# Kernel tuning notes

Measured on AMD Instinct MI355X. Metric: run time of the kernel, lower is better.

## Reference

```python
import jax, jax.numpy as jnp
import numpy as np

B, S, D, H = 4, 2048, 1024, 16
DK = D // H


def setup_inputs() -> dict:
    key = jax.random.key(0)
    ks = jax.random.split(key, 12)
    std = 0.02
    inp = {
        "q": jax.random.normal(ks[0], (B, S, D), jnp.float32),
        "k": jax.random.normal(ks[1], (B, S, D), jnp.float32),
        "v": jax.random.normal(ks[2], (B, S, D), jnp.float32),
        # causal mask: 1 above diagonal (positions to be masked with -inf)
        "mask": jnp.triu(jnp.ones((S, S), jnp.int32), k=1)[None, None, :, :],
        "Wq": jax.random.normal(ks[3], (D, D), jnp.float32) * std,
        "bq": jnp.zeros((D,), jnp.float32),
        "Wk": jax.random.normal(ks[4], (D, D), jnp.float32) * std,
        "bk": jnp.zeros((D,), jnp.float32),
        "Wv": jax.random.normal(ks[5], (D, D), jnp.float32) * std,
        "bv": jnp.zeros((D,), jnp.float32),
        "Wo": jax.random.normal(ks[6], (D, D), jnp.float32) * std,
        "bo": jnp.zeros((D,), jnp.float32),
    }
    return inp


def _split_heads(x):
    b, s, d = x.shape
    return x.reshape(b, s, H, DK).transpose(0, 2, 1, 3)  # [B,H,S,DK]


def reference(q, k, v, mask, Wq, bq, Wk, bk, Wv, bv, Wo, bo):
    # linear projections (torch Linear: x @ W.T + b)
    qh = _split_heads(q @ Wq.T + bq)
    kh = _split_heads(k @ Wk.T + bk)
    vh = _split_heads(v @ Wv.T + bv)
    scale = 1.0 / jnp.sqrt(jnp.asarray(DK, qh.dtype))
    scores = jnp.einsum("bhqd,bhkd->bhqk", qh, kh) * scale
    scores = jnp.where(mask == 1, -jnp.inf, scores)
    attn = jax.nn.softmax(scores, axis=-1)
    # dropout is identity in eval mode (deterministic reference)
    out = jnp.einsum("bhqk,bhkd->bhqd", attn, vh)
    concat = out.transpose(0, 2, 1, 3).reshape(q.shape[0], -1, D)
    return concat @ Wo.T + bo
```

## Files before the change

kernel.cpp:

```cpp
#include <hip/hip_runtime.h>
#include <hip/hip_bf16.h>

#define BB  4
#define SS  2048
#define DD  1024
#define HH  16
#define DKK 64

typedef unsigned short u16;
typedef short v8s __attribute__((ext_vector_type(8)));
typedef short v4s __attribute__((ext_vector_type(4)));
typedef float v4f __attribute__((ext_vector_type(4)));
typedef float v16f __attribute__((ext_vector_type(16)));
typedef unsigned int v4u __attribute__((ext_vector_type(4)));

#define MFMA32(a, b, c) __builtin_amdgcn_mfma_f32_32x32x16_bf16(a, b, c, 0, 0, 0)

__device__ __forceinline__ u16 f2b(float x) {
  unsigned int u = __float_as_uint(x);
  unsigned int r = (u + 0x7fffu + ((u >> 16) & 1u)) >> 16;
  return (u16)r;
}

__device__ __forceinline__ unsigned int pkhalf(float a, float b) {
  return __builtin_amdgcn_perm(__float_as_uint(a), __float_as_uint(b), 0x03020706u);
}

__device__ __forceinline__ void gload16(const u16* g, u16* l) {
  __builtin_amdgcn_global_load_lds(
      (const __attribute__((address_space(1))) void*)g,
      (__attribute__((address_space(3))) void*)l, 16, 0, 0);
}

__device__ __forceinline__ void cvt8(const float* in, u16* out, size_t j) {
  const float4* p = (const float4*)(in + j * 8);
  float4 a = p[0], b = p[1];
  v8s r = {(short)f2b(a.x), (short)f2b(a.y), (short)f2b(a.z), (short)f2b(a.w),
           (short)f2b(b.x), (short)f2b(b.y), (short)f2b(b.z), (short)f2b(b.w)};
  *(v8s*)(out + j * 8) = r;
}

__global__ void cvt3(const float* __restrict__ q, const float* __restrict__ k,
                     const float* __restrict__ v, u16* __restrict__ x0,
                     u16* __restrict__ x1, u16* __restrict__ x2) {
  int i = blockIdx.x * blockDim.x + threadIdx.x;
  int which = i >> 20;
  size_t j = (size_t)(i & 0xFFFFF);
  const float* s = which == 0 ? q : (which == 1 ? k : v);
  u16* d = which == 0 ? x0 : (which == 1 ? x1 : x2);
  cvt8(s, d, j);
}

__global__ void cvtW(const float* __restrict__ a, const float* __restrict__ b,
                     const float* __restrict__ c, const float* __restrict__ d,
                     u16* __restrict__ oa, u16* __restrict__ ob,
                     u16* __restrict__ oc, u16* __restrict__ od) {
  int i = blockIdx.x * blockDim.x + threadIdx.x;
  int which = i >> 17;
  size_t j = (size_t)(i & 0x1FFFF);
  const float* s = which == 0 ? a : (which == 1 ? b : (which == 2 ? c : d));
  u16* o = which == 0 ? oa : (which == 1 ? ob : (which == 2 ? oc : od));
  cvt8(s, o, j);
}

__device__ __forceinline__ void gemm_core32(
    const u16* __restrict__ A, const u16* __restrict__ Bw,
    int row0, int col0, u16* As, u16* Bs, v4f acc[4][4]) {
  const int tid = threadIdx.x;
  const int lane = tid & 63, wid = tid >> 6;
  const int wm = wid >> 1, wn = wid & 1;
  const int lr = lane & 15, lg = lane >> 4;

  v4f zero = {0.f, 0.f, 0.f, 0.f};
#pragma unroll
  for (int m = 0; m < 4; ++m)
#pragma unroll
    for (int n = 0; n < 4; ++n) acc[m][n] = zero;

  const int srow = wid * 16 + (lane >> 2);
  const int scol = ((lane & 3) ^ ((lane >> 3) & 3)) * 8;
  const u16* gA = A + (size_t)(row0 + srow) * DD + scol;
  const u16* gB = Bw + (size_t)(col0 + srow) * DD + scol;
  u16* lA = As + wid * 512;
  u16* lB = Bs + wid * 512;

#pragma unroll
  for (int i2 = 0; i2 < 2; ++i2) {
    gload16(gA + (size_t)(i2 * 64) * DD, lA + i2 * 2048);
    gload16(gB + (size_t)(i2 * 64) * DD, lB + i2 * 2048);
  }
  asm volatile("s_waitcnt vmcnt(0)" ::: "memory");
  __builtin_amdgcn_s_barrier();

  const int aswz = (lg ^ ((lr >> 1) & 3)) * 8;

  for (int t = 0; t < 32; ++t) {
    const int buf = t & 1;
    if (t < 31) {
#pragma unroll
      for (int i2 = 0; i2 < 2; ++i2) {
        gload16(gA + (size_t)(i2 * 64) * DD + (t + 1) * 32,
                lA + (buf ^ 1) * 4096 + i2 * 2048);
        gload16(gB + (size_t)(i2 * 64) * DD + (t + 1) * 32,
                lB + (buf ^ 1) * 4096 + i2 * 2048);
      }
    }
    const u16* Ab = As + buf * 4096;
    const u16* Bb = Bs + buf * 4096;
    v8s af[4], bf[4];
#pragma unroll
    for (int m = 0; m < 4; ++m)
      af[m] = *(const v8s*)(Ab + (wm * 64 + m * 16 + lr) * 32 + aswz);
#pragma unroll
    for (int n = 0; n < 4; ++n)
      bf[n] = *(const v8s*)(Bb + (wn * 64 + n * 16 + lr) * 32 + aswz);
#pragma unroll
    for (int m = 0; m < 4; ++m)
#pragma unroll
      for (int n = 0; n < 4; ++n)
        acc[m][n] = __builtin_amdgcn_mfma_f32_16x16x32_bf16(af[m], bf[n], acc[m][n], 0, 0, 0);

    asm volatile("s_waitcnt vmcnt(0)" ::: "memory");
    __builtin_amdgcn_s_barrier();
  }
}

__global__ __launch_bounds__(256) void gemm_qkv(
    const u16* __restrict__ X0, const u16* __restrict__ X1, const u16* __restrict__ X2,
    const u16* __restrict__ Wqb, const u16* __restrict__ Wkb, const u16* __restrict__ Wvb,
    const float* __restrict__ bq, const float* __restrict__ bk, const float* __restrict__ bv,
    u16* __restrict__ Qp, u16* __restrict__ Kp, u16* __restrict__ VT, float qsc) {
  __shared__ u16 As[2][128][32];
  __shared__ u16 Bs[2][128][32];
  const int z = blockIdx.z;
  const u16* A = z == 0 ? X0 : (z == 1 ? X1 : X2);
  const u16* Bw = z == 0 ? Wqb : (z == 1 ? Wkb : Wvb);
  const float* bias = z == 0 ? bq : (z == 1 ? bk : bv);
  const float oscale = z == 0 ? qsc : 1.0f;
  const int row0 = blockIdx.x * 128, col0 = blockIdx.y * 128;

  v4f acc[4][4];
  gemm_core32(A, Bw, row0, col0, &As[0][0][0], &Bs[0][0][0], acc);

  const int tid = threadIdx.x;
  const int lane = tid & 63, wid = tid >> 6;
  const int wm = wid >> 1, wn = wid & 1;
  const int lr = lane & 15, lg = lane >> 4;

  if (z < 2) {
    u16* C = z == 0 ? Qp : Kp;
#pragma unroll
    for (int n = 0; n < 4; ++n) {
      int gc = col0 + wn * 64 + n * 16 + lr;
      float bv2 = bias[gc];
#pragma unroll
      for (int m = 0; m < 4; ++m) {
        int gr0 = row0 + wm * 64 + m * 16 + lg * 4;
#pragma unroll
        for (int r = 0; r < 4; ++r)
          C[(size_t)(gr0 + r) * DD + gc] = f2b((acc[m][n][r] + bv2) * oscale);
      }
    }
  } else {
#pragma unroll
    for (int n = 0; n < 4; ++n) {
      int gc = col0 + wn * 64 + n * 16 + lr;
      float bv2 = bias[gc];
      int h = gc >> 6, dk = gc & 63;
#pragma unroll
      for (int m = 0; m < 4; ++m) {
        int gr0 = row0 + wm * 64 + m * 16 + lg * 4;
        int b = gr0 >> 11;
        int s = gr0 & 2047;
        u16* vbase = VT + (((size_t)b * HH + h) * DKK + dk) * SS + s;
#pragma unroll
        for (int r = 0; r < 4; ++r) vbase[r] = f2b(acc[m][n][r] + bv2);
      }
    }
  }
}

__global__ __launch_bounds__(256) void gemm_out(
    const u16* __restrict__ A, const u16* __restrict__ Bw,
    const float* __restrict__ bias, float* __restrict__ Cp) {
  __shared__ u16 As[2][128][32];
  __shared__ u16 Bs[2][128][32];
  const int row0 = blockIdx.x * 128, col0 = blockIdx.y * 128;

  v4f acc[4][4];
  gemm_core32(A, Bw, row0, col0, &As[0][0][0], &Bs[0][0][0], acc);

  const int tid = threadIdx.x;
  const int lane = tid & 63, wid = tid >> 6;
  const int wm = wid >> 1, wn = wid & 1;
  const int lr = lane & 15, lg = lane >> 4;

#pragma unroll
  for (int n = 0; n < 4; ++n) {
    int gc = col0 + wn * 64 + n * 16 + lr;
    float bv2 = bias[gc];
#pragma unroll
    for (int m = 0; m < 4; ++m) {
      int gr0 = row0 + wm * 64 + m * 16 + lg * 4;
#pragma unroll
      for (int r = 0; r < 4; ++r)
        Cp[(size_t)(gr0 + r) * DD + gc] = acc[m][n][r] + bv2;
    }
  }
}

__device__ __forceinline__ void build_pa(const v16f& p, int hi, v8s& a0, v8s& a1) {
  unsigned int u0 = pkhalf(p[0], p[1]);
  unsigned int u1 = pkhalf(p[2], p[3]);
  unsigned int u2 = pkhalf(p[4], p[5]);
  unsigned int u3 = pkhalf(p[6], p[7]);
  unsigned int u4 = pkhalf(p[8], p[9]);
  unsigned int u5 = pkhalf(p[10], p[11]);
  unsigned int u6 = pkhalf(p[12], p[13]);
  unsigned int u7 = pkhalf(p[14], p[15]);
  unsigned int s0 = hi ? u0 : u2;
  unsigned int s1 = hi ? u1 : u3;
  unsigned int s2 = hi ? u4 : u6;
  unsigned int s3 = hi ? u5 : u7;
  unsigned int r0 = __shfl_xor(s0, 32);
  unsigned int r1 = __shfl_xor(s1, 32);
  unsigned int r2 = __shfl_xor(s2, 32);
  unsigned int r3 = __shfl_xor(s3, 32);
  v4u f0 = {hi ? r0 : u0, hi ? r1 : u1, hi ? u2 : r0, hi ? u3 : r1};
  v4u f1 = {hi ? r2 : u4, hi ? r3 : u5, hi ? u6 : r2, hi ? u7 : r3};
  a0 = __builtin_bit_cast(v8s, f0);
  a1 = __builtin_bit_cast(v8s, f1);
}

__global__ __launch_bounds__(256) void attn_fwd5(
    const u16* __restrict__ Qp, const u16* __restrict__ Kp,
    const u16* __restrict__ VT, u16* __restrict__ O) {
  __shared__ u16 Ks[128][72];
  __shared__ u16 Vs[64][136];
  const int tid = threadIdx.x;
  const int w = tid >> 6, lane = tid & 63;
  const int ql = lane & 31;
  const int hi = lane >> 5;
  const int i = blockIdx.x;
  const int dw = i >> 8, sl2 = i & 255;
  const int bh = sl2 & 63, g = sl2 >> 6;
  const int qt = (int)((0x3210674598BACDEFull >> (4 * (dw * 4 + g))) & 15);
  const int b = bh >> 4, h = bh & 15;
  const int q0 = qt * 128;
  const int qw0 = q0 + w * 32;
  const int qg = qw0 + ql;

  v8s qf[4];
  const u16* qbase = Qp + (size_t)(b * SS + qg) * DD + h * DKK + hi * 8;
#pragma unroll
  for (int ks = 0; ks < 4; ++ks) qf[ks] = *(const v8s*)(qbase + ks * 16);

  const int krow = tid >> 3, kcol = (tid & 7) * 8;
  const int vrow = tid >> 4, vcol = (tid & 15) * 8;
  const u16* gK = Kp + (size_t)(b * SS + krow) * DD + h * DKK + kcol;
  const u16* gV = VT + ((size_t)bh * DKK + vrow) * SS + vcol;

  const int nt = qt + 1;
  v8s stK[4], stV[4];
#pragma unroll
  for (int j = 0; j < 4; ++j) stK[j] = *(const v8s*)(gK + (size_t)(32 * j) * DD);
#pragma unroll
  for (int j = 0; j < 4; ++j) stV[j] = *(const v8s*)(gV + (size_t)(16 * j) * SS);

  float l = 0.f;
  v16f o0 = {0, 0, 0, 0, 0, 0, 0, 0, 0, 0, 0, 0, 0, 0, 0, 0};
  v16f o1 = o0;

  for (int t = 0; t < nt; ++t) {
    __syncthreads();
#pragma unroll
    for (int j = 0; j < 4; ++j) *(v8s*)&Ks[krow + 32 * j][kcol] = stK[j];
#pragma unroll
    for (int j = 0; j < 4; ++j) *(v8s*)&Vs[vrow + 16 * j][vcol] = stV[j];
    if (t + 1 < nt) {
      const u16* nK = gK + (size_t)(t + 1) * 128 * DD;
      const u16* nV = gV + (t + 1) * 128;
#pragma unroll
      for (int j = 0; j < 4; ++j) stK[j] = *(const v8s*)(nK + (size_t)(32 * j) * DD);
#pragma unroll
      for (int j = 0; j < 4; ++j) stV[j] = *(const v8s*)(nV + (size_t)(16 * j) * SS);
    }
    __syncthreads();
    const int kv0 = t * 128;

#pragma unroll
    for (int sub = 0; sub < 4; ++sub) {
      const int kvs = kv0 + sub * 32;
      if (kvs > qw0 + 31) break;

      v16f p = {0, 0, 0, 0, 0, 0, 0, 0, 0, 0, 0, 0, 0, 0, 0, 0};
#pragma unroll
      for (int ks = 0; ks < 4; ++ks) {
        v8s a = *(const v8s*)&Ks[sub * 32 + ql][ks * 16 + hi * 8];
        p = MFMA32(a, qf[ks], p);
      }

      if (kvs + 31 > qw0) {
#pragma unroll
        for (int r = 0; r < 16; ++r) {
          int row = (r & 3) + 8 * (r >> 2) + 4 * hi;
          if (kvs + row > qg) p[r] = -3.0e38f;
        }
      }

      float rs = 0.f;
#pragma unroll
      for (int r = 0; r < 16; ++r) {
        p[r] = exp2f(p[r]);
        rs += p[r];
      }
      l += rs;

      v8s pa0, pa1;
      build_pa(p, hi, pa0, pa1);

      __builtin_amdgcn_s_setprio(1);
      o0 = MFMA32(pa0, *(const v8s*)&Vs[ql][sub * 32 + hi * 8], o0);
      o0 = MFMA32(pa1, *(const v8s*)&Vs[ql][sub * 32 + 16 + hi * 8], o0);
      o1 = MFMA32(pa0, *(const v8s*)&Vs[32 + ql][sub * 32 + hi * 8], o1);
      o1 = MFMA32(pa1, *(const v8s*)&Vs[32 + ql][sub * 32 + 16 + hi * 8], o1);
      __builtin_amdgcn_s_setprio(0);
    }
  }

  float lt = l + __shfl_xor(l, 32);
  float linv = 1.f / lt;
#pragma unroll
  for (int r = 0; r < 16; ++r) {
    int row = (r & 3) + 8 * (r >> 2) + 4 * hi;
    float lr2 = __shfl(linv, row);
    size_t obase = (size_t)(b * SS + qw0 + row) * DD + h * DKK + ql;
    O[obase] = f2b(o0[r] * lr2);
    O[obase + 32] = f2b(o1[r] * lr2);
  }
}

extern "C" void kernel_launch(void* const* d_in, const int* in_sizes, int n_in,
                              void* d_out, int out_size, void* d_ws, size_t ws_size,
                              hipStream_t stream) {
  (void)in_sizes; (void)n_in; (void)out_size; (void)ws_size;
  const float* q  = (const float*)d_in[0];
  const float* k  = (const float*)d_in[1];
  const float* v  = (const float*)d_in[2];
  const float* Wq = (const float*)d_in[4];
  const float* bq = (const float*)d_in[5];
  const float* Wk = (const float*)d_in[6];
  const float* bk = (const float*)d_in[7];
  const float* Wv = (const float*)d_in[8];
  const float* bv = (const float*)d_in[9];
  const float* Wo = (const float*)d_in[10];
  const float* bo = (const float*)d_in[11];

  u16* base = (u16*)d_ws;
  const size_t WE = (size_t)DD * DD;
  const size_t PE = (size_t)BB * SS * DD;
  u16* Wq_b = base;
  u16* Wk_b = Wq_b + WE;
  u16* Wv_b = Wk_b + WE;
  u16* Wo_b = Wv_b + WE;
  u16* Qp = Wo_b + WE;
  u16* Kp = Qp + PE;
  u16* X2 = Kp + PE;
  u16* VT = X2 + PE;
  u16* Op = X2;

  u16* X0 = (u16*)d_out;
  u16* X1 = X0 + PE;

  const float qsc = 0.125f * 1.44269504f;

  cvtW<<<2048, 256, 0, stream>>>(Wq, Wk, Wv, Wo, Wq_b, Wk_b, Wv_b, Wo_b);
  cvt3<<<12288, 256, 0, stream>>>(q, k, v, X0, X1, X2);

  dim3 gq(64, 8, 3);
  gemm_qkv<<<gq, 256, 0, stream>>>(X0, X1, X2, Wq_b, Wk_b, Wv_b,
                                   bq, bk, bv, Qp, Kp, VT, qsc);

  attn_fwd5<<<1024, 256, 0, stream>>>(Qp, Kp, VT, Op);

  dim3 go(64, 8);
  gemm_out<<<go, 256, 0, stream>>>(Op, Wo_b, bo, (float*)d_out);
}
```

Before: 219.3 us.

## Fuse fp32-to-bf16 input conversion into QKV projection GEMM

Removes the separate cvt3 kernel that converted q/k/v activations to bf16. The QKV GEMM now streams fp32 activation tiles straight into LDS with swizzled direct loads and converts them to bf16 while building MFMA fragments. This saves a kernel launch plus a full write and re-read of the bf16 activations. In exchange it doubles the LDS footprint and global traffic for the A operand inside the GEMM, and it adds per-iteration conversion ALU work that is repeated across the 8 column blocks.

```diff
diff --git a/kernel.cpp b/kernel.cpp
--- a/kernel.cpp
+++ b/kernel.cpp
@@ -9,7 +9,7 @@
 
 typedef unsigned short u16;
 typedef short v8s __attribute__((ext_vector_type(8)));
-typedef short v4s __attribute__((ext_vector_type(4)));
+typedef float f32x4 __attribute__((ext_vector_type(4)));
 typedef float v4f __attribute__((ext_vector_type(4)));
 typedef float v16f __attribute__((ext_vector_type(16)));
 typedef unsigned int v4u __attribute__((ext_vector_type(4)));
@@ -27,6 +27,11 @@
 }
 
 __device__ __forceinline__ void gload16(const u16* g, u16* l) {
+  __builtin_amdgcn_global_load_lds(
+      (const __attribute__((address_space(1))) void*)g,
+      (__attribute__((address_space(3))) void*)l, 16, 0, 0);
+}
+__device__ __forceinline__ void gload16f(const float* g, float* l) {
   __builtin_amdgcn_global_load_lds(
       (const __attribute__((address_space(1))) void*)g,
       (__attribute__((address_space(3))) void*)l, 16, 0, 0);
@@ -38,17 +43,6 @@
   v8s r = {(short)f2b(a.x), (short)f2b(a.y), (short)f2b(a.z), (short)f2b(a.w),
            (short)f2b(b.x), (short)f2b(b.y), (short)f2b(b.z), (short)f2b(b.w)};
   *(v8s*)(out + j * 8) = r;
-}
-
-__global__ void cvt3(const float* __restrict__ q, const float* __restrict__ k,
-                     const float* __restrict__ v, u16* __restrict__ x0,
-                     u16* __restrict__ x1, u16* __restrict__ x2) {
-  int i = blockIdx.x * blockDim.x + threadIdx.x;
-  int which = i >> 20;
-  size_t j = (size_t)(i & 0xFFFFF);
-  const float* s = which == 0 ? q : (which == 1 ? k : v);
-  u16* d = which == 0 ? x0 : (which == 1 ? x1 : x2);
-  cvt8(s, d, j);
 }
 
 __global__ void cvtW(const float* __restrict__ a, const float* __restrict__ b,
@@ -63,6 +57,124 @@
   cvt8(s, o, j);
 }
 
+__global__ __launch_bounds__(256) void gemm_qkvf2(
+    const float* __restrict__ Xq, const float* __restrict__ Xk, const float* __restrict__ Xv,
+    const u16* __restrict__ Wqb, const u16* __restrict__ Wkb, const u16* __restrict__ Wvb,
+    const float* __restrict__ bq, const float* __restrict__ bk, const float* __restrict__ bv,
+    u16* __restrict__ Qp, u16* __restrict__ Kp, u16* __restrict__ VT, float qsc) {
+  __shared__ float Af[2][128][32];
+  __shared__ u16 Bs[2][128][32];
+  const int z = blockIdx.z;
+  const float* A = z == 0 ? Xq : (z == 1 ? Xk : Xv);
+  const u16* Bw = z == 0 ? Wqb : (z == 1 ? Wkb : Wvb);
+  const float* bias = z == 0 ? bq : (z == 1 ? bk : bv);
+  const float oscale = z == 0 ? qsc : 1.0f;
+  const int row0 = blockIdx.x * 128, col0 = blockIdx.y * 128;
+
+  const int tid = threadIdx.x;
+  const int lane = tid & 63, wid = tid >> 6;
+  const int wm = wid >> 1, wn = wid & 1;
+  const int lr = lane & 15, lg = lane >> 4;
+
+  v4f zero = {0.f, 0.f, 0.f, 0.f};
+  v4f acc[4][4];
+#pragma unroll
+  for (int m = 0; m < 4; ++m)
+#pragma unroll
+    for (int n = 0; n < 4; ++n) acc[m][n] = zero;
+
+  const int arow = tid >> 3;
+  const int agc = (tid & 7) ^ ((tid >> 3) & 7);
+  const float* gAf = A + (size_t)(row0 + arow) * DD + agc * 4;
+  float* lA = &Af[0][0][0] + wid * 256;
+
+  const int bsrow = wid * 16 + (lane >> 2);
+  const int bscol = ((lane & 3) ^ ((lane >> 3) & 3)) * 8;
+  const u16* gB = Bw + (size_t)(col0 + bsrow) * DD + bscol;
+  u16* lB = &Bs[0][0][0] + wid * 512;
+
+#pragma unroll
+  for (int i2 = 0; i2 < 4; ++i2)
+    gload16f(gAf + (size_t)(i2 * 32) * DD, lA + i2 * 1024);
+#pragma unroll
+  for (int i2 = 0; i2 < 2; ++i2)
+    gload16(gB + (size_t)(i2 * 64) * DD, lB + i2 * 2048);
+  asm volatile("s_waitcnt vmcnt(0)" ::: "memory");
+  __builtin_amdgcn_s_barrier();
+
+  const int s0 = (2 * lg) ^ (lr & 7);
+  const int bswz = (lg ^ ((lr >> 1) & 3)) * 8;
+
+  for (int t = 0; t < 32; ++t) {
+    const int buf = t & 1;
+    if (t < 31) {
+#pragma unroll
+      for (int i2 = 0; i2 < 4; ++i2)
+        gload16f(gAf + (size_t)(i2 * 32) * DD + (t + 1) * 32,
+                 lA + (buf ^ 1) * 4096 + i2 * 1024);
+#pragma unroll
+      for (int i2 = 0; i2 < 2; ++i2)
+        gload16(gB + (size_t)(i2 * 64) * DD + (t + 1) * 32,
+                lB + (buf ^ 1) * 4096 + i2 * 2048);
+    }
+    const float* Ab = &Af[buf][0][0];
+    const u16* Bb = &Bs[buf][0][0];
+    v8s af[4], bf[4];
+#pragma unroll
+    for (int m = 0; m < 4; ++m) {
+      const int rr = wm * 64 + m * 16 + lr;
+      f32x4 a0 = *(const f32x4*)(Ab + rr * 32 + s0 * 4);
+      f32x4 a1 = *(const f32x4*)(Ab + rr * 32 + (s0 ^ 1) * 4);
+      v8s fr = {(short)f2b(a0[0]), (short)f2b(a0[1]), (short)f2b(a0[2]), (short)f2b(a0[3]),
+                (short)f2b(a1[0]), (short)f2b(a1[1]), (short)f2b(a1[2]), (short)f2b(a1[3])};
+      af[m] = fr;
+    }
+#pragma unroll
+    for (int n = 0; n < 4; ++n)
+      bf[n] = *(const v8s*)(Bb + (wn * 64 + n * 16 + lr) * 32 + bswz);
+#pragma unroll
+    for (int m = 0; m < 4; ++m)
+#pragma unroll
+      for (int n = 0; n < 4; ++n)
+        acc[m][n] = __builtin_amdgcn_mfma_f32_16x16x32_bf16(af[m], bf[n], acc[m][n], 0, 0, 0);
+
+    asm volatile("s_waitcnt vmcnt(0)" ::: "memory");
+    __builtin_amdgcn_s_barrier();
+  }
+
+  if (z < 2) {
+    u16* C = z == 0 ? Qp : Kp;
+#pragma unroll
+    for (int n = 0; n < 4; ++n) {
+      int gc = col0 + wn * 64 + n * 16 + lr;
+      float bv2 = bias[gc];
+#pragma unroll
+      for (int m = 0; m < 4; ++m) {
+        int gr0 = row0 + wm * 64 + m * 16 + lg * 4;
+#pragma unroll
+        for (int r = 0; r < 4; ++r)
+          C[(size_t)(gr0 + r) * DD + gc] = f2b((acc[m][n][r] + bv2) * oscale);
+      }
+    }
+  } else {
+#pragma unroll
+    for (int n = 0; n < 4; ++n) {
+      int gc = col0 + wn * 64 + n * 16 + lr;
+      float bv2 = bias[gc];
+      int h = gc >> 6, dk = gc & 63;
+#pragma unroll
+      for (int m = 0; m < 4; ++m) {
+        int gr0 = row0 + wm * 64 + m * 16 + lg * 4;
+        int b = gr0 >> 11;
+        int s = gr0 & 2047;
+        u16* vbase = VT + (((size_t)b * HH + h) * DKK + dk) * SS + s;
+#pragma unroll
+        for (int r = 0; r < 4; ++r) vbase[r] = f2b(acc[m][n][r] + bv2);
+      }
+    }
+  }
+}
+
 __device__ __forceinline__ void gemm_core32(
     const u16* __restrict__ A, const u16* __restrict__ Bw,
     int row0, int col0, u16* As, u16* Bs, v4f acc[4][4]) {
@@ -122,61 +234,6 @@
 
     asm volatile("s_waitcnt vmcnt(0)" ::: "memory");
     __builtin_amdgcn_s_barrier();
-  }
-}
-
-__global__ __launch_bounds__(256) void gemm_qkv(
-    const u16* __restrict__ X0, const u16* __restrict__ X1, const u16* __restrict__ X2,
-    const u16* __restrict__ Wqb, const u16* __restrict__ Wkb, const u16* __restrict__ Wvb,
-    const float* __restrict__ bq, const float* __restrict__ bk, const float* __restrict__ bv,
-    u16* __restrict__ Qp, u16* __restrict__ Kp, u16* __restrict__ VT, float qsc) {
-  __shared__ u16 As[2][128][32];
-  __shared__ u16 Bs[2][128][32];
-  const int z = blockIdx.z;
-  const u16* A = z == 0 ? X0 : (z == 1 ? X1 : X2);
-  const u16* Bw = z == 0 ? Wqb : (z == 1 ? Wkb : Wvb);
-  const float* bias = z == 0 ? bq : (z == 1 ? bk : bv);
-  const float oscale = z == 0 ? qsc : 1.0f;
-  const int row0 = blockIdx.x * 128, col0 = blockIdx.y * 128;
-
-  v4f acc[4][4];
-  gemm_core32(A, Bw, row0, col0, &As[0][0][0], &Bs[0][0][0], acc);
-
-  const int tid = threadIdx.x;
-  const int lane = tid & 63, wid = tid >> 6;
-  const int wm = wid >> 1, wn = wid & 1;
-  const int lr = lane & 15, lg = lane >> 4;
-
-  if (z < 2) {
-    u16* C = z == 0 ? Qp : Kp;
-#pragma unroll
-    for (int n = 0; n < 4; ++n) {
-      int gc = col0 + wn * 64 + n * 16 + lr;
-      float bv2 = bias[gc];
-#pragma unroll
-      for (int m = 0; m < 4; ++m) {
-        int gr0 = row0 + wm * 64 + m * 16 + lg * 4;
-#pragma unroll
-        for (int r = 0; r < 4; ++r)
-          C[(size_t)(gr0 + r) * DD + gc] = f2b((acc[m][n][r] + bv2) * oscale);
-      }
-    }
-  } else {
-#pragma unroll
-    for (int n = 0; n < 4; ++n) {
-      int gc = col0 + wn * 64 + n * 16 + lr;
-      float bv2 = bias[gc];
-      int h = gc >> 6, dk = gc & 63;
-#pragma unroll
-      for (int m = 0; m < 4; ++m) {
-        int gr0 = row0 + wm * 64 + m * 16 + lg * 4;
-        int b = gr0 >> 11;
-        int s = gr0 & 2047;
-        u16* vbase = VT + (((size_t)b * HH + h) * DKK + dk) * SS + s;
-#pragma unroll
-        for (int r = 0; r < 4; ++r) vbase[r] = f2b(acc[m][n][r] + bv2);
-      }
-    }
   }
 }
 
@@ -365,21 +422,16 @@
   u16* Wo_b = Wv_b + WE;
   u16* Qp = Wo_b + WE;
   u16* Kp = Qp + PE;
-  u16* X2 = Kp + PE;
-  u16* VT = X2 + PE;
-  u16* Op = X2;
-
-  u16* X0 = (u16*)d_out;
-  u16* X1 = X0 + PE;
+  u16* VT = Kp + PE;
+  u16* Op = VT + PE;
 
   const float qsc = 0.125f * 1.44269504f;
 
   cvtW<<<2048, 256, 0, stream>>>(Wq, Wk, Wv, Wo, Wq_b, Wk_b, Wv_b, Wo_b);
-  cvt3<<<12288, 256, 0, stream>>>(q, k, v, X0, X1, X2);
 
   dim3 gq(64, 8, 3);
-  gemm_qkv<<<gq, 256, 0, stream>>>(X0, X1, X2, Wq_b, Wk_b, Wv_b,
-                                   bq, bk, bv, Qp, Kp, VT, qsc);
+  gemm_qkvf2<<<gq, 256, 0, stream>>>(q, k, v, Wq_b, Wk_b, Wv_b,
+                                     bq, bk, bv, Qp, Kp, VT, qsc);
 
   attn_fwd5<<<1024, 256, 0, stream>>>(Qp, Kp, VT, Op);
 
```

Measured after the change: 235.0 us. +7.2%, slower.
